# Kernel tuning notes

Hardware: AMD Instinct MI355X
Metric: run time of the kernel (lower is better)

## Reference

```python
import jax, jax.numpy as jnp
import numpy as np

N_HOPS = 6
NEG_INF = -1e30


def setup_inputs() -> dict:
    key = jax.random.key(0)
    ks = jax.random.split(key, 12)
    B, L, T, V, D, C = 64, 512, 8, 50000, 1024, 3
    context_ids = jax.random.randint(ks[0], (B, L), 0, V, dtype=jnp.int32)
    target_ids = jax.random.randint(ks[1], (B, T), 0, V, dtype=jnp.int32)
    context_len = jax.random.randint(ks[2], (B,), 256, L + 1, dtype=jnp.int32)
    target_len = jax.random.randint(ks[3], (B,), 2, T + 1, dtype=jnp.int32)
    target_offset = jax.random.randint(ks[4], (B,), 0, 256, dtype=jnp.int32)
    s = 0.02
    return {
        "context_ids": context_ids,
        "target_ids": target_ids,
        "context_len": context_len,
        "target_len": target_len,
        "target_offset": target_offset,
        "embedding_matrix": jax.random.normal(ks[5], (V, D), jnp.float32) * s,
        "W_lin": jax.random.normal(ks[6], (D, D), jnp.float32) * s,
        "b_lin": jax.random.normal(ks[7], (D,), jnp.float32) * s,
        "w_attn": jax.random.normal(ks[8], (2 * D, 1), jnp.float32) * s,
        "b_attn": jax.random.normal(ks[9], (1,), jnp.float32) * s,
        "W_out": jax.random.normal(ks[10], (D, C), jnp.float32) * s,
        "b_out": jax.random.normal(ks[11], (C,), jnp.float32) * s,
    }


def reference(context_ids, target_ids, context_len, target_len, target_offset,
              embedding_matrix, W_lin, b_lin, w_attn, b_attn, W_out, b_out):
    B, L = context_ids.shape
    T = target_ids.shape[1]

    pos = jnp.arange(L, dtype=jnp.int32)[None, :]            # [1,L]
    ctx_mask = pos < context_len[:, None]                    # [B,L] valid positions

    # location model 2: v_i = 1 - |i - target_offset| / seq_len, zeroed off-sequence
    dist = jnp.abs(pos - target_offset[:, None]).astype(jnp.float32)
    v_loc = (1.0 - dist / context_len[:, None].astype(jnp.float32))
    v_loc = jnp.where(ctx_mask, v_loc, 0.0)                  # [B,L]

    memory = embedding_matrix[context_ids]                   # [B,L,D]
    ext_memory = memory * v_loc[..., None]                   # [B,L,D] (loc-model-2 branch)

    # v_aspect: variable-length mean of target embeddings
    tgt_emb = embedding_matrix[target_ids]                   # [B,T,D]
    t_mask = (jnp.arange(T, dtype=jnp.int32)[None, :] < target_len[:, None])
    v_aspect = (tgt_emb * t_mask[..., None].astype(jnp.float32)).sum(axis=1)
    v_aspect = v_aspect / target_len[:, None].astype(jnp.float32)  # [B,D]

    vec = v_aspect
    for _ in range(N_HOPS):  # fixed hop count; linear + attn params shared (AUTO_REUSE)
        lin = vec @ W_lin + b_lin                            # [B,D]
        # content attention: tanh(W [m_i ; v] + b) scores
        s_mem = jnp.einsum('bld,dk->bl', ext_memory, w_attn[: ext_memory.shape[-1]])
        s_vec = vec @ w_attn[ext_memory.shape[-1]:]          # [B,1]
        scores = jnp.tanh(s_mem + s_vec + b_attn[0])         # [B,L]
        scores = jnp.where(ctx_mask, scores, NEG_INF)
        alpha = jax.nn.softmax(scores, axis=-1)              # [B,L]
        attn_out = jnp.einsum('bl,bld->bd', alpha, ext_memory)
        vec = attn_out + lin

    logits = vec @ W_out + b_out                             # [B,C]
    return logits
```

## Files before the change

kernel.cpp:

```cpp
#include <hip/hip_runtime.h>
#include <cstdint>


#define DD 1024
#define LL 512
#define BB 64
#define MTS 32

__global__ __launch_bounds__(256) void k_init(const float* __restrict__ w_attn,
                                              const float* __restrict__ W_out,
                                              float* __restrict__ Mt,
                                              float* __restrict__ Mc)
{
  int d = blockIdx.x * 256 + threadIdx.x;
  float w0 = w_attn[d];
  float u0 = w_attn[DD + d];
  Mt[d * MTS + 0] = w0; Mc[0 * DD + d] = w0;
  Mt[d * MTS + 1] = u0; Mc[1 * DD + d] = u0;
#pragma unroll
  for (int c = 0; c < 3; ++c) {
    float y = W_out[d * 3 + c];
    int col = 7 + 6 * c;
    Mt[d * MTS + col] = y; Mc[col * DD + d] = y;
  }
}

__global__ __launch_bounds__(256) void k_chain(const float* __restrict__ Wl,
                                               float* __restrict__ Mt,
                                               float* __restrict__ Mc,
                                               int i0, int i1, int i2, int i3,
                                               int o0, int o1, int o2, int o3)
{
  int tid = threadIdx.x;
  int wv = __builtin_amdgcn_readfirstlane(tid >> 6);
  int ln = tid & 63;
  int i = blockIdx.x * 4 + wv;
  const float* wrow = Wl + (size_t)i * DD;
  int c0 = i0 < 0 ? 0 : i0, c1 = i1 < 0 ? 0 : i1;
  int c2 = i2 < 0 ? 0 : i2, c3 = i3 < 0 ? 0 : i3;
  float s0 = 0.f, s1 = 0.f, s2 = 0.f, s3 = 0.f;
  for (int m = 0; m < 16; ++m) {
    int j = ln + m * 64;
    float w = wrow[j];
    s0 += w * Mc[c0 * DD + j];
    s1 += w * Mc[c1 * DD + j];
    s2 += w * Mc[c2 * DD + j];
    s3 += w * Mc[c3 * DD + j];
  }
#pragma unroll
  for (int m = 1; m < 64; m <<= 1) {
    s0 += __shfl_xor(s0, m, 64); s1 += __shfl_xor(s1, m, 64);
    s2 += __shfl_xor(s2, m, 64); s3 += __shfl_xor(s3, m, 64);
  }
  if (ln == 0) {
    if (o0 >= 0) { Mt[i * MTS + o0] = s0; Mc[o0 * DD + i] = s0; }
    if (o1 >= 0) { Mt[i * MTS + o1] = s1; Mc[o1 * DD + i] = s1; }
    if (o2 >= 0) { Mt[i * MTS + o2] = s2; Mc[o2 * DD + i] = s2; }
    if (o3 >= 0) { Mt[i * MTS + o3] = s3; Mc[o3 * DD + i] = s3; }
  }
}

__global__ __launch_bounds__(256, 2) void k_gemm(const int* __restrict__ ctx_ids,
                                                 const int* __restrict__ ctx_len,
                                                 const int* __restrict__ toff,
                                                 const float* __restrict__ emb,
                                                 const float* __restrict__ Mt,
                                                 float* __restrict__ Q)
{
  __shared__ float stag[4][64 * 33];
  __shared__ float qp[4][64][25];
  int tid = threadIdx.x;
  int kq = __builtin_amdgcn_readfirstlane(tid >> 6);
  int ln = tid & 63;
  int rowbase = blockIdx.x * 64;
  int myid = ctx_ids[rowbase + ln];
  const float* base[8];
#pragma unroll
  for (int ii = 0; ii < 8; ++ii) {
    int rid = __shfl(myid, ii * 8 + (ln >> 3), 64);
    base[ii] = emb + (size_t)rid * DD;
  }
  int p4 = (ln & 7) * 4;
  float* sw = stag[kq];
  int k0 = kq * 256;
  float acc[25];
#pragma unroll
  for (int j = 0; j < 25; ++j) acc[j] = 0.f;

  float4 buf[2][8];
#pragma unroll
  for (int ii = 0; ii < 8; ++ii)
    buf[0][ii] = *(const float4*)(base[ii] + k0 + p4);
#pragma unroll
  for (int ii = 0; ii < 8; ++ii)
    buf[1][ii] = *(const float4*)(base[ii] + k0 + 32 + p4);

  for (int ch = 0; ch < 8; ++ch) {
    int cur = ch & 1;
#pragma unroll
    for (int ii = 0; ii < 8; ++ii) {
      int r = ii * 8 + (ln >> 3);
      int a = r * 33 + p4;
      sw[a + 0] = buf[cur][ii].x; sw[a + 1] = buf[cur][ii].y;
      sw[a + 2] = buf[cur][ii].z; sw[a + 3] = buf[cur][ii].w;
    }
    if (ch < 6) {
      int kb = k0 + (ch + 2) * 32;
#pragma unroll
      for (int ii = 0; ii < 8; ++ii)
        buf[cur][ii] = *(const float4*)(base[ii] + kb + p4);
    }
    __builtin_amdgcn_s_waitcnt(0xc07f);
    const float* mrow = Mt + (size_t)(k0 + ch * 32) * MTS;
#pragma unroll 4
    for (int kk = 0; kk < 32; ++kk) {
      float mv = sw[ln * 33 + kk];
#pragma unroll
      for (int j = 0; j < 25; ++j) acc[j] += mv * mrow[kk * MTS + j];
    }
  }
#pragma unroll
  for (int j = 0; j < 25; ++j) qp[kq][ln][j] = acc[j];
  __syncthreads();

  int b = rowbase >> 9;
  int l0 = rowbase & 511;
  int clen = ctx_len[b];
  int off = toff[b];
  float fclen = (float)clen;
  for (int i = tid; i < 1600; i += 256) {
    int j = i >> 6, r = i & 63;
    float s = qp[0][r][j] + qp[1][r][j] + qp[2][r][j] + qp[3][r][j];
    int l = l0 + r;
    float vl = (l < clen) ? (1.f - fabsf((float)(l - off)) / fclen) : 0.f;
    Q[((size_t)b * 25 + j) * LL + l] = s * vl;
  }
}

template <bool ISMAX, int NW>
__device__ __forceinline__ void breduce(float* v, int n, float* lds, int tid)
{
  int wv = __builtin_amdgcn_readfirstlane(tid >> 6);
  int ln = tid & 63;
  for (int q = 0; q < n; ++q) {
    float x = v[q];
#pragma unroll
    for (int m = 1; m < 64; m <<= 1) {
      float o = __shfl_xor(x, m, 64);
      x = ISMAX ? fmaxf(x, o) : x + o;
    }
    if (ln == 0) lds[q * NW + wv] = x;
  }
  __syncthreads();
  for (int q = 0; q < n; ++q) {
    float r = lds[q * NW + 0];
#pragma unroll
    for (int w = 1; w < NW; ++w)
      r = ISMAX ? fmaxf(r, lds[q * NW + w]) : r + lds[q * NW + w];
    v[q] = r;
  }
  __syncthreads();
}

__global__ __launch_bounds__(512) void k_hop(const int* __restrict__ tgt_ids,
                                             const int* __restrict__ tgt_len,
                                             const int* __restrict__ ctx_len,
                                             const float* __restrict__ emb,
                                             const float* __restrict__ b_lin,
                                             const float* __restrict__ b_attn,
                                             const float* __restrict__ b_out,
                                             const float* __restrict__ Mc,
                                             const float* __restrict__ Q,
                                             float* __restrict__ out)
{
  __shared__ float Qs[25 * LL];
  __shared__ float va[DD];
  __shared__ float red[32 * 8];
  int tid = threadIdx.x;
  int b = blockIdx.x;

  {
    const float4* src = (const float4*)(Q + (size_t)b * (25 * LL));
    float4* dst = (float4*)Qs;
    for (int i = tid; i < 25 * LL / 4; i += 512) dst[i] = src[i];
  }

  int tl = tgt_len[b];
  float inv_tl = 1.f / (float)tl;
  for (int d = tid; d < DD; d += 512) {
    float s = 0.f;
#pragma unroll
    for (int t = 0; t < 8; ++t)
      if (t < tl) s += emb[(size_t)tgt_ids[b * 8 + t] * DD + d];
    va[d] = s * inv_tl;
  }
  __syncthreads();

  float p[32];
#pragma unroll
  for (int q = 0; q < 32; ++q) p[q] = 0.f;
  for (int d = tid; d < DD; d += 512) {
    float vad = va[d], bd = b_lin[d];
#pragma unroll
    for (int k = 0; k < 6; ++k) {
      float u = Mc[(1 + k) * DD + d];
      p[k] += vad * u;
      if (k < 5) p[9 + k] += bd * u;
    }
#pragma unroll
    for (int c = 0; c < 3; ++c) {
      p[6 + c] += vad * Mc[(25 + c) * DD + d];
#pragma unroll
      for (int k = 0; k < 6; ++k)
        p[14 + c * 6 + k] += bd * Mc[(7 + 6 * c + k) * DD + d];
    }
  }
  breduce<false, 8>(p, 32, red, tid);

  float tcur[6], rc[3], beta[5], gam[18];
#pragma unroll
  for (int k = 0; k < 6; ++k) tcur[k] = p[k];
#pragma unroll
  for (int c = 0; c < 3; ++c) rc[c] = p[6 + c];
#pragma unroll
  for (int k = 0; k < 5; ++k) beta[k] = p[9 + k];
#pragma unroll
  for (int q = 0; q < 18; ++q) gam[q] = p[14 + q];

  int clen = ctx_len[b];
  float batt = b_attn[0];
  bool act = tid < clen;

  for (int h = 0; h < 6; ++h) {
    float pe[9];
#pragma unroll
    for (int q = 0; q < 9; ++q) pe[q] = 0.f;
    int kd = 5 - h;
    if (act) {
      float e = expf(tanhf(Qs[tid] + tcur[0] + batt));
      pe[0] = e;
      for (int k = 0; k <= 4 - h; ++k) pe[1 + k] = e * Qs[(1 + k) * LL + tid];
#pragma unroll
      for (int c = 0; c < 3; ++c) pe[6 + c] = e * Qs[(7 + 6 * c + kd) * LL + tid];
    }
    breduce<false, 8>(pe, 9, red, tid);

    float invS = 1.f / pe[0];
    for (int k = 0; k <= 4 - h; ++k)
      tcur[k] = pe[1 + k] * invS + tcur[k + 1] + beta[k];
#pragma unroll
    for (int c = 0; c < 3; ++c)
      rc[c] = pe[6 + c] * invS + rc[c] + gam[c * 6 + kd];
  }
  if (tid < 3) out[b * 3 + tid] = rc[tid] + b_out[tid];
}

extern "C" void kernel_launch(void* const* d_in, const int* in_sizes, int n_in,
                              void* d_out, int out_size, void* d_ws, size_t ws_size,
                              hipStream_t stream)
{
  const int*   ctx_ids = (const int*)d_in[0];
  const int*   tgt_ids = (const int*)d_in[1];
  const int*   ctx_len = (const int*)d_in[2];
  const int*   tgt_len = (const int*)d_in[3];
  const int*   toff    = (const int*)d_in[4];
  const float* emb     = (const float*)d_in[5];
  const float* Wl      = (const float*)d_in[6];
  const float* bl      = (const float*)d_in[7];
  const float* wat     = (const float*)d_in[8];
  const float* bat     = (const float*)d_in[9];
  const float* Wo      = (const float*)d_in[10];
  const float* bo      = (const float*)d_in[11];
  float* ws = (float*)d_ws;
  float* Mt = ws;
  float* Mc = ws + 32768;
  float* Q  = ws + 65536;
  float* outp = (float*)d_out;

  hipLaunchKernelGGL(k_init, dim3(4), dim3(256), 0, stream, wat, Wo, Mt, Mc);
  for (int s = 1; s <= 6; ++s) {
    int i0 = (s <= 5) ? s : -1;
    int o0 = (s <= 5) ? (1 + s) : -1;
    int i1 = 6 + s,  o1 = (s <= 5) ? (7 + s)  : 25;
    int i2 = 12 + s, o2 = (s <= 5) ? (13 + s) : 26;
    int i3 = 18 + s, o3 = (s <= 5) ? (19 + s) : 27;
    hipLaunchKernelGGL(k_chain, dim3(256), dim3(256), 0, stream,
                       Wl, Mt, Mc, i0, i1, i2, i3, o0, o1, o2, o3);
  }
  hipLaunchKernelGGL(k_gemm, dim3(512), dim3(256), 0, stream,
                     ctx_ids, ctx_len, toff, emb, Mt, Q);
  hipLaunchKernelGGL(k_hop, dim3(64), dim3(512), 0, stream,
                     tgt_ids, tgt_len, ctx_len, emb, bl, bat, bo, Mc, Q, outp);
}
```

Baseline: 363.5 us.

## Load embedding rows directly per lane in gather GEMM, dropping LDS staging

Restructures the gather-GEMM kernel so each lane reads its own embedding row with float4 loads from global memory, replacing the cooperative LDS-transposed staging. The block grows to 512 threads, with 8 waves each covering a 128-wide K slice, and the partial sums are reduced across 8 slices. This removes LDS writes and reads and the waitcnt stalls. In exchange, each lane's loads are strided by a full row and no longer coalesced across the wave, and there is a larger cross-wave reduction.

```diff
diff --git a/kernel.cpp b/kernel.cpp
--- a/kernel.cpp
+++ b/kernel.cpp
@@ -60,65 +60,46 @@
   }
 }
 
-__global__ __launch_bounds__(256, 2) void k_gemm(const int* __restrict__ ctx_ids,
+__global__ __launch_bounds__(512, 1) void k_gemm(const int* __restrict__ ctx_ids,
                                                  const int* __restrict__ ctx_len,
                                                  const int* __restrict__ toff,
                                                  const float* __restrict__ emb,
                                                  const float* __restrict__ Mt,
                                                  float* __restrict__ Q)
 {
-  __shared__ float stag[4][64 * 33];
-  __shared__ float qp[4][64][25];
+  __shared__ float qp[8][64][25];
   int tid = threadIdx.x;
   int kq = __builtin_amdgcn_readfirstlane(tid >> 6);
   int ln = tid & 63;
   int rowbase = blockIdx.x * 64;
-  int myid = ctx_ids[rowbase + ln];
-  const float* base[8];
-#pragma unroll
-  for (int ii = 0; ii < 8; ++ii) {
-    int rid = __shfl(myid, ii * 8 + (ln >> 3), 64);
-    base[ii] = emb + (size_t)rid * DD;
-  }
-  int p4 = (ln & 7) * 4;
-  float* sw = stag[kq];
-  int k0 = kq * 256;
+  int rid = ctx_ids[rowbase + ln];
+  const float* rp = emb + (size_t)rid * DD + kq * 128;
+  const float* mt = Mt + (size_t)(kq * 128) * MTS;
+
   float acc[25];
 #pragma unroll
   for (int j = 0; j < 25; ++j) acc[j] = 0.f;
 
-  float4 buf[2][8];
-#pragma unroll
-  for (int ii = 0; ii < 8; ++ii)
-    buf[0][ii] = *(const float4*)(base[ii] + k0 + p4);
-#pragma unroll
-  for (int ii = 0; ii < 8; ++ii)
-    buf[1][ii] = *(const float4*)(base[ii] + k0 + 32 + p4);
-
-  for (int ch = 0; ch < 8; ++ch) {
-    int cur = ch & 1;
-#pragma unroll
-    for (int ii = 0; ii < 8; ++ii) {
-      int r = ii * 8 + (ln >> 3);
-      int a = r * 33 + p4;
-      sw[a + 0] = buf[cur][ii].x; sw[a + 1] = buf[cur][ii].y;
-      sw[a + 2] = buf[cur][ii].z; sw[a + 3] = buf[cur][ii].w;
-    }
-    if (ch < 6) {
-      int kb = k0 + (ch + 2) * 32;
-#pragma unroll
-      for (int ii = 0; ii < 8; ++ii)
-        buf[cur][ii] = *(const float4*)(base[ii] + kb + p4);
-    }
-    __builtin_amdgcn_s_waitcnt(0xc07f);
-    const float* mrow = Mt + (size_t)(k0 + ch * 32) * MTS;
-#pragma unroll 4
-    for (int kk = 0; kk < 32; ++kk) {
-      float mv = sw[ln * 33 + kk];
-#pragma unroll
-      for (int j = 0; j < 25; ++j) acc[j] += mv * mrow[kk * MTS + j];
-    }
-  }
+  float4 v[8];
+#pragma unroll
+  for (int u = 0; u < 8; ++u) v[u] = *(const float4*)(rp + u * 4);
+
+  for (int c = 0; c < 32; c += 8) {
+#pragma unroll
+    for (int u = 0; u < 8; ++u) {
+      float4 x = v[u];
+      if (c + 8 + u < 32) v[u] = *(const float4*)(rp + (c + 8 + u) * 4);
+      const float* m = mt + (size_t)(c + u) * 4 * MTS;
+#pragma unroll
+      for (int j = 0; j < 25; ++j) {
+        acc[j] += x.x * m[j];
+        acc[j] += x.y * m[MTS + j];
+        acc[j] += x.z * m[2 * MTS + j];
+        acc[j] += x.w * m[3 * MTS + j];
+      }
+    }
+  }
+
 #pragma unroll
   for (int j = 0; j < 25; ++j) qp[kq][ln][j] = acc[j];
   __syncthreads();
@@ -128,9 +109,11 @@
   int clen = ctx_len[b];
   int off = toff[b];
   float fclen = (float)clen;
-  for (int i = tid; i < 1600; i += 256) {
+  for (int i = tid; i < 1600; i += 512) {
     int j = i >> 6, r = i & 63;
-    float s = qp[0][r][j] + qp[1][r][j] + qp[2][r][j] + qp[3][r][j];
+    float s = 0.f;
+#pragma unroll
+    for (int w = 0; w < 8; ++w) s += qp[w][r][j];
     int l = l0 + r;
     float vl = (l < clen) ? (1.f - fabsf((float)(l - off)) / fclen) : 0.f;
     Q[((size_t)b * 25 + j) * LL + l] = s * vl;
@@ -287,7 +270,7 @@
     hipLaunchKernelGGL(k_chain, dim3(256), dim3(256), 0, stream,
                        Wl, Mt, Mc, i0, i1, i2, i3, o0, o1, o2, o3);
   }
-  hipLaunchKernelGGL(k_gemm, dim3(512), dim3(256), 0, stream,
+  hipLaunchKernelGGL(k_gemm, dim3(512), dim3(512), 0, stream,
                      ctx_ids, ctx_len, toff, emb, Mt, Q);
   hipLaunchKernelGGL(k_hop, dim3(64), dim3(512), 0, stream,
                      tgt_ids, tgt_len, ctx_len, emb, bl, bat, bo, Mc, Q, outp);
```

Result: slower. 400.6 us (+10.2%).
